# Optimization experiments

Hardware: AMD Instinct MI355X
Metric: run time of the kernel (lower is better)

Reference implementation:

```python
import jax, jax.numpy as jnp
import numpy as np

EMBED = 1024
BATCH = 512
K_STEPS = 96


def setup_inputs() -> dict:
    key = jax.random.key(0)
    ks = jax.random.split(key, 5)
    s = 1.0 / np.sqrt(EMBED)  # PyTorch GRU init scale
    return {
        "c": jax.random.normal(ks[0], (BATCH, EMBED), dtype=jnp.float32),
        "K": K_STEPS,
        "W_ih": jax.random.uniform(ks[1], (3 * EMBED, EMBED), minval=-s, maxval=s, dtype=jnp.float32),
        "W_hh": jax.random.uniform(ks[2], (3 * EMBED, EMBED), minval=-s, maxval=s, dtype=jnp.float32),
        "b_ih": jax.random.uniform(ks[3], (3 * EMBED,), minval=-s, maxval=s, dtype=jnp.float32),
        "b_hh": jax.random.uniform(ks[4], (3 * EMBED,), minval=-s, maxval=s, dtype=jnp.float32),
    }


def _gru_step(x, h, W_ih, W_hh, b_ih, b_hh):
    # PyTorch GRU gate order: reset, update, new
    gi = x @ W_ih.T + b_ih  # [B, 3H]
    gh = h @ W_hh.T + b_hh  # [B, 3H]
    i_r, i_z, i_n = jnp.split(gi, 3, axis=-1)
    h_r, h_z, h_n = jnp.split(gh, 3, axis=-1)
    r = jax.nn.sigmoid(i_r + h_r)
    z = jax.nn.sigmoid(i_z + h_z)
    n = jnp.tanh(i_n + r * h_n)
    return (1.0 - z) * n + z * h  # new hidden == output (seq_len=1)


def reference(c, K, W_ih, W_hh, b_ih, b_hh):
    B = c.shape[0]
    x0 = jnp.zeros((B, EMBED), dtype=c.dtype)

    def step(carry, _):
        x, h = carry
        h_new = _gru_step(x, h, W_ih, W_hh, b_ih, b_hh)
        # output y_k == h_new is fed back as next input x_{k+1}
        return (h_new, h_new), h_new

    _, ys = jax.lax.scan(step, (x0, c), None, length=K)  # ys: [K, B, H]
    return jnp.transpose(ys, (1, 0, 2))  # [B, K, H]
```

## Files before the change

kernel.cpp:

```cpp
#include <hip/hip_runtime.h>
#include <math.h>

#define H 1024
#define BATCH 512
#define KSTEPS 96
#define KH ((long)KSTEPS * H)

typedef __attribute__((ext_vector_type(8))) short short8;
typedef __attribute__((ext_vector_type(16))) float f32x16;

__device__ __forceinline__ unsigned short f2bf(float x) {
    union { float f; unsigned int u; } v; v.f = x;
    unsigned int r = v.u + 0x7fffu + ((v.u >> 16) & 1u);
    return (unsigned short)(r >> 16);
}

__device__ __forceinline__ float fsig(float x)  { return 1.f / (1.f + __expf(-x)); }
__device__ __forceinline__ float ftanh(float x) { return 1.f - 2.f / (1.f + __expf(2.f * x)); }

#define MEMFENCE asm volatile("" ::: "memory")


__global__ void prep_w(const float* __restrict__ wih,
                       const float* __restrict__ whh,
                       unsigned short* __restrict__ blob0,
                       unsigned short* __restrict__ blob1)
{
    const unsigned int f = blockIdx.x * 256 + threadIdx.x;
    const int e  = f & 7;
    const int l  = (f >> 3) & 63;
    const int kg = (f >> 9) & 1;
    const int js = (f >> 10) & 3;
    const int Jt = (f >> 12) & 31;
    const int tc = (f >> 17) & 31;
    const int b  = blockIdx.y;

    const int J = Jt * 128 + js * 32 + (l & 31);
    const int g = J & 3;
    const long j = J >> 2;
    const long k = (long)tc * 32 + kg * 16 + (l >> 5) * 8 + e;

    float v = 0.f;
    if (b == 1) {
        if (g == 0)      v = wih[j*1024 + k]           + whh[j*1024 + k];
        else if (g == 1) v = wih[(1024+j)*1024 + k]    + whh[(1024+j)*1024 + k];
        else if (g == 2) v = wih[(2048+j)*1024 + k];
        else             v = whh[(2048+j)*1024 + k];
    } else {
        if (g == 0)      v = whh[j*1024 + k];
        else if (g == 1) v = whh[(1024+j)*1024 + k];
        else if (g == 2) v = 0.f;
        else             v = whh[(2048+j)*1024 + k];
    }
    unsigned short* blob = (b == 0) ? blob0 : blob1;
    blob[f] = f2bf(v);
}

__global__ void prep_bcJ(const float* __restrict__ bih,
                         const float* __restrict__ bhh,
                         float* __restrict__ bcJ,
                         unsigned int* __restrict__ bar)
{
    const int J = blockIdx.x * 256 + threadIdx.x;
    const int g = J & 3;
    const int j = J >> 2;
    float v;
    if (g == 0)      v = bih[j]        + bhh[j];
    else if (g == 1) v = bih[1024 + j] + bhh[1024 + j];
    else if (g == 2) v = bih[2048 + j];
    else             v = bhh[2048 + j];
    bcJ[J] = v;
    if (blockIdx.x == 0) {
        bar[threadIdx.x]       = 0u;
        bar[256 + threadIdx.x] = 0u;
    }
}

__global__ void prep_h0(const float* __restrict__ cin,
                        unsigned short* __restrict__ hT)
{
    const unsigned int f = blockIdx.x * 256 + threadIdx.x;
    const int e  = f & 7;
    const int l  = (f >> 3) & 63;
    const int kg = (f >> 9) & 1;
    const int mh = (f >> 10) & 1;
    const int cc = (f >> 11) & 15;
    const int ph = (f >> 15) & 1;
    const int mt = (f >> 16) & 7;

    const long m = mt * 64 + mh * 32 + (l & 31);
    const long k = (long)(ph * 16 + cc) * 32 + kg * 16 + (l >> 5) * 8 + e;

    hT[f] = f2bf(cin[m * 1024 + k]);
}

__global__ __launch_bounds__(512) void gru_all(
    const unsigned short* __restrict__ blob0,
    const unsigned short* __restrict__ blob1,
    unsigned short* __restrict__ hTa,
    unsigned short* __restrict__ hTb,
    const float* __restrict__ cin,
    const float* __restrict__ bcJ,
    float* __restrict__ out,
    unsigned int* bar)
{
    __shared__ __attribute__((aligned(16))) char smem[65536 + 8 * 9232];

    const int tid  = threadIdx.x;
    const int lane = tid & 63;
    const int wv   = tid >> 6;
    const int kg   = wv & 1;
    const int js   = wv >> 1;

    const int id   = blockIdx.x;
    const int grp  = id & 7;
    const int slot = id >> 3;
    const int Jt   = grp * 4 + (slot & 3);
    const int mt   = slot >> 2;

    const float bias = (kg == 0) ? bcJ[Jt * 128 + js * 32 + (lane & 31)] : 0.f;

    char*  ldsA  = smem;
    float* Dbase = (float*)(smem + 65536);
    float* Dp    = Dbase + (js * 2 + kg) * 2308;

    float hp[4];
    #pragma unroll
    for (int q = 0; q < 4; ++q) {
        const int qi = q * 512 + tid;
        const int jl = qi & 31;
        const int m  = qi >> 5;
        hp[q] = cin[((long)mt * 64 + m) * 1024 + (long)Jt * 32 + jl];
    }

    #pragma unroll 1
    for (int k = 0; k < KSTEPS; ++k) {
        const unsigned short* blob = (k == 0) ? blob0 : blob1;
        const char* wbase = (const char*)blob + (long)(Jt * 8 + js * 2 + kg) * 1024;
        const unsigned short* hTr = (k & 1) ? hTb : hTa;
        unsigned short*       hTw = (k & 1) ? hTa : hTb;
        const char* hbase = (const char*)hTr + (long)mt * 131072;
        float* outk = out + (long)k * H;

        short8 W0, W1, W2;

        auto loadW = [&](int c, short8& Wd) {
            const char* p = wbase + (long)c * 262144;
            asm volatile("global_load_dwordx4 %0, %1, off"
                         : "=v"(Wd) : "v"(p + lane * 16) : "memory");
        };
        auto stageA = [&](int ph, bool drainAll) {
            const char* src = hbase + ph * 65536;
            short8 t0, t1, t2, t3, t4, t5, t6, t7;
            asm volatile("global_load_dwordx4 %0, %1, off sc0 sc1" : "=v"(t0) : "v"(src + (0*512 + tid)*16) : "memory");
            asm volatile("global_load_dwordx4 %0, %1, off sc0 sc1" : "=v"(t1) : "v"(src + (1*512 + tid)*16) : "memory");
            asm volatile("global_load_dwordx4 %0, %1, off sc0 sc1" : "=v"(t2) : "v"(src + (2*512 + tid)*16) : "memory");
            asm volatile("global_load_dwordx4 %0, %1, off sc0 sc1" : "=v"(t3) : "v"(src + (3*512 + tid)*16) : "memory");
            asm volatile("global_load_dwordx4 %0, %1, off sc0 sc1" : "=v"(t4) : "v"(src + (4*512 + tid)*16) : "memory");
            asm volatile("global_load_dwordx4 %0, %1, off sc0 sc1" : "=v"(t5) : "v"(src + (5*512 + tid)*16) : "memory");
            asm volatile("global_load_dwordx4 %0, %1, off sc0 sc1" : "=v"(t6) : "v"(src + (6*512 + tid)*16) : "memory");
            asm volatile("global_load_dwordx4 %0, %1, off sc0 sc1" : "=v"(t7) : "v"(src + (7*512 + tid)*16) : "memory");
            if (drainAll) asm volatile("s_waitcnt vmcnt(0)" ::: "memory");
            else          asm volatile("s_waitcnt vmcnt(3)" ::: "memory");
            __builtin_amdgcn_sched_barrier(0);
            *(short8*)(ldsA + (0*512 + tid)*16) = t0;
            *(short8*)(ldsA + (1*512 + tid)*16) = t1;
            *(short8*)(ldsA + (2*512 + tid)*16) = t2;
            *(short8*)(ldsA + (3*512 + tid)*16) = t3;
            *(short8*)(ldsA + (4*512 + tid)*16) = t4;
            *(short8*)(ldsA + (5*512 + tid)*16) = t5;
            *(short8*)(ldsA + (6*512 + tid)*16) = t6;
            *(short8*)(ldsA + (7*512 + tid)*16) = t7;
            asm volatile("s_waitcnt lgkmcnt(0)" ::: "memory");
        };

        f32x16 accLo, accHi;
        #pragma unroll
        for (int r = 0; r < 16; ++r) { accLo[r] = bias; accHi[r] = 0.f; }
        if (kg == 0) {
            #pragma unroll
            for (int r = 0; r < 16; ++r) accHi[r] = bias;
        }

        if (k > 0) {
            if (wv == 0 && lane < 32) {
                unsigned int* fp = bar + (mt * 32 + lane);
                while (true) {
                    unsigned v;
                    asm volatile("global_load_dword %0, %1, off sc0 sc1\n\t"
                                 "s_waitcnt vmcnt(0)"
                                 : "=v"(v) : "v"(fp) : "memory");
                    if (v >= (unsigned)k) break;
                    __builtin_amdgcn_s_sleep(2);
                }
            }
        }
        __syncthreads();

        {
            const char* src = hbase;
        }
        {
            const char* src = hbase;
            short8 t0, t1, t2, t3, t4, t5, t6, t7;
            asm volatile("global_load_dwordx4 %0, %1, off sc0 sc1" : "=v"(t0) : "v"(src + (0*512 + tid)*16) : "memory");
            asm volatile("global_load_dwordx4 %0, %1, off sc0 sc1" : "=v"(t1) : "v"(src + (1*512 + tid)*16) : "memory");
            asm volatile("global_load_dwordx4 %0, %1, off sc0 sc1" : "=v"(t2) : "v"(src + (2*512 + tid)*16) : "memory");
            asm volatile("global_load_dwordx4 %0, %1, off sc0 sc1" : "=v"(t3) : "v"(src + (3*512 + tid)*16) : "memory");
            asm volatile("global_load_dwordx4 %0, %1, off sc0 sc1" : "=v"(t4) : "v"(src + (4*512 + tid)*16) : "memory");
            asm volatile("global_load_dwordx4 %0, %1, off sc0 sc1" : "=v"(t5) : "v"(src + (5*512 + tid)*16) : "memory");
            asm volatile("global_load_dwordx4 %0, %1, off sc0 sc1" : "=v"(t6) : "v"(src + (6*512 + tid)*16) : "memory");
            asm volatile("global_load_dwordx4 %0, %1, off sc0 sc1" : "=v"(t7) : "v"(src + (7*512 + tid)*16) : "memory");
            loadW(0, W0); loadW(1, W1); loadW(2, W2);
            asm volatile("s_waitcnt vmcnt(3)" ::: "memory");
            __builtin_amdgcn_sched_barrier(0);
            *(short8*)(ldsA + (0*512 + tid)*16) = t0;
            *(short8*)(ldsA + (1*512 + tid)*16) = t1;
            *(short8*)(ldsA + (2*512 + tid)*16) = t2;
            *(short8*)(ldsA + (3*512 + tid)*16) = t3;
            *(short8*)(ldsA + (4*512 + tid)*16) = t4;
            *(short8*)(ldsA + (5*512 + tid)*16) = t5;
            *(short8*)(ldsA + (6*512 + tid)*16) = t6;
            *(short8*)(ldsA + (7*512 + tid)*16) = t7;
            asm volatile("s_waitcnt lgkmcnt(0)" ::: "memory");
        }
        __builtin_amdgcn_s_barrier();

        #define CHUNK(c, N, Wc, Wn)                                            \
        {                                                                      \
            asm volatile("s_waitcnt vmcnt(" #N ")" ::: "memory");              \
            __builtin_amdgcn_sched_barrier(0);                                 \
            const short8 aLo = *(const short8*)(ldsA + (((c)&15)*4 + kg)*1024 + lane*16);     \
            const short8 aHi = *(const short8*)(ldsA + (((c)&15)*4 + 2 + kg)*1024 + lane*16); \
            accLo = __builtin_amdgcn_mfma_f32_32x32x16_bf16(aLo, Wc, accLo, 0, 0, 0); \
            accHi = __builtin_amdgcn_mfma_f32_32x32x16_bf16(aHi, Wc, accHi, 0, 0, 0); \
            if ((c) + 3 < 32) loadW((c) + 3, Wn);                              \
        }

        CHUNK(0,2,W0,W0)  CHUNK(1,2,W1,W1)  CHUNK(2,2,W2,W2)  CHUNK(3,2,W0,W0)
        CHUNK(4,2,W1,W1)  CHUNK(5,2,W2,W2)  CHUNK(6,2,W0,W0)  CHUNK(7,2,W1,W1)
        CHUNK(8,2,W2,W2)  CHUNK(9,2,W0,W0)  CHUNK(10,2,W1,W1) CHUNK(11,2,W2,W2)
        CHUNK(12,2,W0,W0) CHUNK(13,2,W1,W1) CHUNK(14,2,W2,W2) CHUNK(15,2,W0,W0)

        __builtin_amdgcn_s_barrier();
        stageA(1, true);
        __builtin_amdgcn_s_barrier();

        CHUNK(16,2,W1,W1) CHUNK(17,2,W2,W2) CHUNK(18,2,W0,W0) CHUNK(19,2,W1,W1)
        CHUNK(20,2,W2,W2) CHUNK(21,2,W0,W0) CHUNK(22,2,W1,W1) CHUNK(23,2,W2,W2)
        CHUNK(24,2,W0,W0) CHUNK(25,2,W1,W1) CHUNK(26,2,W2,W2) CHUNK(27,2,W0,W0)
        CHUNK(28,2,W1,W1) CHUNK(29,2,W2,W2) CHUNK(30,1,W0,W0) CHUNK(31,0,W1,W1)
        #undef CHUNK

        #pragma unroll
        for (int r = 0; r < 16; ++r) {
            const int r32 = (r & 3) + 8 * (r >> 2) + 4 * (lane >> 5);
            Dp[(r32)      * 36 + (lane & 31)] = accLo[r];
            Dp[(32 + r32) * 36 + (lane & 31)] = accHi[r];
        }
        asm volatile("s_waitcnt lgkmcnt(0)" ::: "memory");
        __builtin_amdgcn_s_barrier();

        #pragma unroll
        for (int q = 0; q < 4; ++q) {
            const int qi = q * 512 + tid;
            const int jl = qi & 31;
            const int m  = qi >> 5;
            const int jsq = jl >> 3;
            const int c4  = (jl & 7) * 4;
            const float4 g0 = *(const float4*)(Dbase + (jsq*2 + 0)*2308 + m*36 + c4);
            const float4 g1 = *(const float4*)(Dbase + (jsq*2 + 1)*2308 + m*36 + c4);
            const float gr = g0.x + g1.x;
            const float gz = g0.y + g1.y;
            const float gi = g0.z + g1.z;
            const float gh = g0.w + g1.w;

            const float rr = fsig(gr);
            const float zz = fsig(gz);
            const float nn = ftanh(fmaf(rr, gh, gi));
            const float o  = nn + zz * (hp[q] - nn);
            hp[q] = o;

            const unsigned short hi = f2bf(o);
            const int j   = Jt * 32 + jl;
            const int c2  = j >> 5;
            const int kg2 = (j >> 4) & 1;
            const int lhi = (j >> 3) & 1;
            const int e2  = j & 7;
            const int ph2 = c2 >> 4;
            const int cc2 = c2 & 15;
            const int mh2 = m >> 5;
            const int l2  = lhi * 32 + (m & 31);
            const long ub = (((((long)mt*2 + ph2)*16 + cc2)*2 + mh2)*2 + kg2)*512
                          + l2*8 + e2;
            unsigned short* p0 = hTw + ub;
            asm volatile("global_store_short %0, %1, off sc0 sc1"
                         :: "v"(p0), "v"((unsigned)hi) : "memory");
        }
        asm volatile("s_waitcnt vmcnt(0)" ::: "memory");
        __builtin_amdgcn_s_barrier();

        if (k < KSTEPS - 1 && tid == 0) {
            const unsigned kk = (unsigned)(k + 1);
            unsigned int* fp = bar + (mt * 32 + Jt);
            asm volatile("global_store_dword %0, %1, off sc0 sc1"
                         :: "v"(fp), "v"(kk) : "memory");
        }
        #pragma unroll
        for (int q = 0; q < 4; ++q) {
            const int qi = q * 512 + tid;
            const int jl = qi & 31;
            const int m  = qi >> 5;
            __builtin_nontemporal_store(hp[q],
                &outk[((long)mt * 64 + m) * KH + (long)Jt * 32 + jl]);
        }
    }
}

extern "C" void kernel_launch(void* const* d_in, const int* in_sizes, int n_in,
                              void* d_out, int out_size, void* d_ws, size_t ws_size,
                              hipStream_t stream)
{
    const float* c   = (const float*)d_in[0];
    const float* wih = (const float*)d_in[2];
    const float* whh = (const float*)d_in[3];
    const float* bih = (const float*)d_in[4];
    const float* bhh = (const float*)d_in[5];
    float* out = (float*)d_out;

    unsigned short* blob0 = (unsigned short*)d_ws;
    unsigned short* blob1 = blob0 + 4194304L;
    float*          bcJ   = (float*)(blob1 + 4194304L);
    unsigned short* hTa   = (unsigned short*)(bcJ + 4096);
    unsigned short* hTb   = hTa + 524288L;
    unsigned int*   bar   = (unsigned int*)(hTb + 524288L);

    prep_w  <<<dim3(16384, 2), 256, 0, stream>>>(wih, whh, blob0, blob1);
    prep_bcJ<<<dim3(16),       256, 0, stream>>>(bih, bhh, bcJ, bar);
    prep_h0 <<<dim3(2048),     256, 0, stream>>>(c, hTa);

    void* args[] = { (void*)&blob0, (void*)&blob1, (void*)&hTa, (void*)&hTb,
                     (void*)&c, (void*)&bcJ, (void*)&out, (void*)&bar };
    hipLaunchCooperativeKernel((const void*)gru_all, dim3(256), dim3(512),
                               args, 0, stream);
}
```

Measured before the change: 816.3 us.

## Stage hidden state into LDS with direct global-to-LDS loads, double-buffered per quarter

Hidden-state staging now uses global_load_lds (direct DMA into LDS) instead of loading into registers and then writing to LDS. The A operand is split into four quarters that are double-buffered in LDS, so the next quarter's load overlaps the MFMA chunks of the current one. This removes the mid-step drain-all stall and weight prefetch now starts before the barrier spin. It also shortens the spin sleep and changes the bias initialisation of accHi. The risks are subtle vmcnt accounting and LDS race errors.

Result: faster. 799.8 us (-2.0%).

```diff
diff --git a/kernel.cpp b/kernel.cpp
--- a/kernel.cpp
+++ b/kernel.cpp
@@ -18,6 +18,11 @@
 __device__ __forceinline__ float fsig(float x)  { return 1.f / (1.f + __expf(-x)); }
 __device__ __forceinline__ float ftanh(float x) { return 1.f - 2.f / (1.f + __expf(2.f * x)); }
 
+__device__ __forceinline__ void glds16(const void* g, void* l) {
+    __builtin_amdgcn_global_load_lds(
+        (const __attribute__((address_space(1))) void*)g,
+        (__attribute__((address_space(3))) void*)l, 16, 0, 0);
+}
 #define MEMFENCE asm volatile("" ::: "memory")
 
 
@@ -149,38 +154,20 @@
             asm volatile("global_load_dwordx4 %0, %1, off"
                          : "=v"(Wd) : "v"(p + lane * 16) : "memory");
         };
-        auto stageA = [&](int ph, bool drainAll) {
-            const char* src = hbase + ph * 65536;
-            short8 t0, t1, t2, t3, t4, t5, t6, t7;
-            asm volatile("global_load_dwordx4 %0, %1, off sc0 sc1" : "=v"(t0) : "v"(src + (0*512 + tid)*16) : "memory");
-            asm volatile("global_load_dwordx4 %0, %1, off sc0 sc1" : "=v"(t1) : "v"(src + (1*512 + tid)*16) : "memory");
-            asm volatile("global_load_dwordx4 %0, %1, off sc0 sc1" : "=v"(t2) : "v"(src + (2*512 + tid)*16) : "memory");
-            asm volatile("global_load_dwordx4 %0, %1, off sc0 sc1" : "=v"(t3) : "v"(src + (3*512 + tid)*16) : "memory");
-            asm volatile("global_load_dwordx4 %0, %1, off sc0 sc1" : "=v"(t4) : "v"(src + (4*512 + tid)*16) : "memory");
-            asm volatile("global_load_dwordx4 %0, %1, off sc0 sc1" : "=v"(t5) : "v"(src + (5*512 + tid)*16) : "memory");
-            asm volatile("global_load_dwordx4 %0, %1, off sc0 sc1" : "=v"(t6) : "v"(src + (6*512 + tid)*16) : "memory");
-            asm volatile("global_load_dwordx4 %0, %1, off sc0 sc1" : "=v"(t7) : "v"(src + (7*512 + tid)*16) : "memory");
-            if (drainAll) asm volatile("s_waitcnt vmcnt(0)" ::: "memory");
-            else          asm volatile("s_waitcnt vmcnt(3)" ::: "memory");
-            __builtin_amdgcn_sched_barrier(0);
-            *(short8*)(ldsA + (0*512 + tid)*16) = t0;
-            *(short8*)(ldsA + (1*512 + tid)*16) = t1;
-            *(short8*)(ldsA + (2*512 + tid)*16) = t2;
-            *(short8*)(ldsA + (3*512 + tid)*16) = t3;
-            *(short8*)(ldsA + (4*512 + tid)*16) = t4;
-            *(short8*)(ldsA + (5*512 + tid)*16) = t5;
-            *(short8*)(ldsA + (6*512 + tid)*16) = t6;
-            *(short8*)(ldsA + (7*512 + tid)*16) = t7;
-            asm volatile("s_waitcnt lgkmcnt(0)" ::: "memory");
+        auto stageAq = [&](int q) {
+            const char* src = hbase + (long)q * 32768 + wv * 4096;
+            char* dst = ldsA + (q & 1) * 32768 + wv * 4096;
+            #pragma unroll
+            for (int i = 0; i < 4; ++i)
+                glds16(src + i * 1024 + lane * 16, dst + i * 1024);
         };
 
         f32x16 accLo, accHi;
         #pragma unroll
-        for (int r = 0; r < 16; ++r) { accLo[r] = bias; accHi[r] = 0.f; }
-        if (kg == 0) {
-            #pragma unroll
-            for (int r = 0; r < 16; ++r) accHi[r] = bias;
-        }
+        for (int r = 0; r < 16; ++r) { accLo[r] = bias; accHi[r] = bias; }
+
+        loadW(0, W0); loadW(1, W1); loadW(2, W2);
+        MEMFENCE;
 
         if (k > 0) {
             if (wv == 0 && lane < 32) {
@@ -191,65 +178,43 @@
                                  "s_waitcnt vmcnt(0)"
                                  : "=v"(v) : "v"(fp) : "memory");
                     if (v >= (unsigned)k) break;
-                    __builtin_amdgcn_s_sleep(2);
+                    __builtin_amdgcn_s_sleep(1);
                 }
             }
         }
         __syncthreads();
 
-        {
-            const char* src = hbase;
-        }
-        {
-            const char* src = hbase;
-            short8 t0, t1, t2, t3, t4, t5, t6, t7;
-            asm volatile("global_load_dwordx4 %0, %1, off sc0 sc1" : "=v"(t0) : "v"(src + (0*512 + tid)*16) : "memory");
-            asm volatile("global_load_dwordx4 %0, %1, off sc0 sc1" : "=v"(t1) : "v"(src + (1*512 + tid)*16) : "memory");
-            asm volatile("global_load_dwordx4 %0, %1, off sc0 sc1" : "=v"(t2) : "v"(src + (2*512 + tid)*16) : "memory");
-            asm volatile("global_load_dwordx4 %0, %1, off sc0 sc1" : "=v"(t3) : "v"(src + (3*512 + tid)*16) : "memory");
-            asm volatile("global_load_dwordx4 %0, %1, off sc0 sc1" : "=v"(t4) : "v"(src + (4*512 + tid)*16) : "memory");
-            asm volatile("global_load_dwordx4 %0, %1, off sc0 sc1" : "=v"(t5) : "v"(src + (5*512 + tid)*16) : "memory");
-            asm volatile("global_load_dwordx4 %0, %1, off sc0 sc1" : "=v"(t6) : "v"(src + (6*512 + tid)*16) : "memory");
-            asm volatile("global_load_dwordx4 %0, %1, off sc0 sc1" : "=v"(t7) : "v"(src + (7*512 + tid)*16) : "memory");
-            loadW(0, W0); loadW(1, W1); loadW(2, W2);
-            asm volatile("s_waitcnt vmcnt(3)" ::: "memory");
-            __builtin_amdgcn_sched_barrier(0);
-            *(short8*)(ldsA + (0*512 + tid)*16) = t0;
-            *(short8*)(ldsA + (1*512 + tid)*16) = t1;
-            *(short8*)(ldsA + (2*512 + tid)*16) = t2;
-            *(short8*)(ldsA + (3*512 + tid)*16) = t3;
-            *(short8*)(ldsA + (4*512 + tid)*16) = t4;
-            *(short8*)(ldsA + (5*512 + tid)*16) = t5;
-            *(short8*)(ldsA + (6*512 + tid)*16) = t6;
-            *(short8*)(ldsA + (7*512 + tid)*16) = t7;
-            asm volatile("s_waitcnt lgkmcnt(0)" ::: "memory");
-        }
-        __builtin_amdgcn_s_barrier();
-
-        #define CHUNK(c, N, Wc, Wn)                                            \
+        stageAq(0);
+        asm volatile("s_waitcnt vmcnt(0)" ::: "memory");
+        __builtin_amdgcn_sched_barrier(0);
+        __builtin_amdgcn_s_barrier();
+
+        #define CHUNK(c, N, Wc, Wn, STG)                                       \
         {                                                                      \
             asm volatile("s_waitcnt vmcnt(" #N ")" ::: "memory");              \
             __builtin_amdgcn_sched_barrier(0);                                 \
-            const short8 aLo = *(const short8*)(ldsA + (((c)&15)*4 + kg)*1024 + lane*16);     \
-            const short8 aHi = *(const short8*)(ldsA + (((c)&15)*4 + 2 + kg)*1024 + lane*16); \
+            const short8 aLo = *(const short8*)(ldsA + (((c)>>3)&1)*32768      \
+                                 + (((c)&7)*4 + kg)*1024 + lane*16);           \
+            const short8 aHi = *(const short8*)(ldsA + (((c)>>3)&1)*32768      \
+                                 + (((c)&7)*4 + 2 + kg)*1024 + lane*16);       \
             accLo = __builtin_amdgcn_mfma_f32_32x32x16_bf16(aLo, Wc, accLo, 0, 0, 0); \
             accHi = __builtin_amdgcn_mfma_f32_32x32x16_bf16(aHi, Wc, accHi, 0, 0, 0); \
             if ((c) + 3 < 32) loadW((c) + 3, Wn);                              \
-        }
-
-        CHUNK(0,2,W0,W0)  CHUNK(1,2,W1,W1)  CHUNK(2,2,W2,W2)  CHUNK(3,2,W0,W0)
-        CHUNK(4,2,W1,W1)  CHUNK(5,2,W2,W2)  CHUNK(6,2,W0,W0)  CHUNK(7,2,W1,W1)
-        CHUNK(8,2,W2,W2)  CHUNK(9,2,W0,W0)  CHUNK(10,2,W1,W1) CHUNK(11,2,W2,W2)
-        CHUNK(12,2,W0,W0) CHUNK(13,2,W1,W1) CHUNK(14,2,W2,W2) CHUNK(15,2,W0,W0)
-
-        __builtin_amdgcn_s_barrier();
-        stageA(1, true);
-        __builtin_amdgcn_s_barrier();
-
-        CHUNK(16,2,W1,W1) CHUNK(17,2,W2,W2) CHUNK(18,2,W0,W0) CHUNK(19,2,W1,W1)
-        CHUNK(20,2,W2,W2) CHUNK(21,2,W0,W0) CHUNK(22,2,W1,W1) CHUNK(23,2,W2,W2)
-        CHUNK(24,2,W0,W0) CHUNK(25,2,W1,W1) CHUNK(26,2,W2,W2) CHUNK(27,2,W0,W0)
-        CHUNK(28,2,W1,W1) CHUNK(29,2,W2,W2) CHUNK(30,1,W0,W0) CHUNK(31,0,W1,W1)
+            if (STG) stageAq(((c) >> 3) + 1);                                  \
+            MEMFENCE;                                                          \
+        }
+
+        CHUNK(0,0,W0,W0,1)  CHUNK(1,6,W1,W1,0)  CHUNK(2,6,W2,W2,0)  CHUNK(3,6,W0,W0,0)
+        CHUNK(4,2,W1,W1,0)  CHUNK(5,2,W2,W2,0)  CHUNK(6,2,W0,W0,0)  CHUNK(7,2,W1,W1,0)
+        __builtin_amdgcn_s_barrier();
+        CHUNK(8,2,W2,W2,1)  CHUNK(9,6,W0,W0,0)  CHUNK(10,6,W1,W1,0) CHUNK(11,6,W2,W2,0)
+        CHUNK(12,2,W0,W0,0) CHUNK(13,2,W1,W1,0) CHUNK(14,2,W2,W2,0) CHUNK(15,2,W0,W0,0)
+        __builtin_amdgcn_s_barrier();
+        CHUNK(16,2,W1,W1,1) CHUNK(17,6,W2,W2,0) CHUNK(18,6,W0,W0,0) CHUNK(19,6,W1,W1,0)
+        CHUNK(20,2,W2,W2,0) CHUNK(21,2,W0,W0,0) CHUNK(22,2,W1,W1,0) CHUNK(23,2,W2,W2,0)
+        __builtin_amdgcn_s_barrier();
+        CHUNK(24,2,W0,W0,0) CHUNK(25,2,W1,W1,0) CHUNK(26,2,W2,W2,0) CHUNK(27,2,W0,W0,0)
+        CHUNK(28,2,W1,W1,0) CHUNK(29,2,W2,W2,0) CHUNK(30,1,W0,W0,0) CHUNK(31,0,W1,W1,0)
         #undef CHUNK
 
         #pragma unroll
```
